# Performance work log

Measured on AMD Instinct MI355X. Metric: run time of the kernel, lower is better.

The kernel has to match this reference:

```python
import jax, jax.numpy as jnp
import numpy as np

N_NODES = 50000


def _build_graph(edge_index):
    # Add self-loops (PyG GCNConv default) and compute symmetric normalization.
    n = N_NODES
    loops = jnp.arange(n, dtype=edge_index.dtype)
    src = jnp.concatenate([edge_index[0], loops])
    dst = jnp.concatenate([edge_index[1], loops])
    deg = jax.ops.segment_sum(jnp.ones_like(dst, dtype=jnp.float32), dst, num_segments=n)
    dinv = jax.lax.rsqrt(jnp.maximum(deg, 1e-12))
    norm = dinv[src] * dinv[dst]  # [E+N]
    return src, dst, norm


def _gcn_layer(h, src, dst, norm, W, b):
    # transform-then-propagate: out[dst] += norm * (h @ W)[src]
    h = h @ W  # [N, D_out]
    msg = h[src] * norm[:, None]  # [E+N, D_out]
    agg = jax.ops.segment_sum(msg, dst, num_segments=N_NODES)
    return agg + b


def setup_inputs() -> dict:
    key = jax.random.key(0)
    ks = jax.random.split(key, 8)
    in_dim, hid, out = 128, 64, 32
    n_edges = 800000
    x = jax.random.normal(ks[0], (N_NODES, in_dim), dtype=jnp.float32)
    edge_index = jax.random.randint(ks[1], (2, n_edges), 0, N_NODES, dtype=jnp.int32)
    W1 = jax.random.normal(ks[2], (in_dim, hid), dtype=jnp.float32) / np.sqrt(in_dim)
    b1 = jnp.zeros((hid,), jnp.float32)
    W2 = jax.random.normal(ks[3], (hid, out), dtype=jnp.float32) / np.sqrt(hid)
    b2 = jnp.zeros((out,), jnp.float32)
    attn_w = jax.random.normal(ks[4], (out, 1), dtype=jnp.float32) / np.sqrt(out)
    attn_b = jnp.zeros((1,), jnp.float32)
    return {"x": x, "edge_index": edge_index, "W1": W1, "b1": b1,
            "W2": W2, "b2": b2, "attn_w": attn_w, "attn_b": attn_b}


def reference(x, edge_index, W1, b1, W2, b2, attn_w, attn_b):
    src, dst, norm = _build_graph(edge_index)
    h = jax.nn.relu(_gcn_layer(x, src, dst, norm, W1, b1))
    h = jax.nn.relu(_gcn_layer(h, src, dst, norm, W2, b2))
    attn = jax.nn.sigmoid(h @ attn_w + attn_b)  # [N, 1]
    return h * attn
```

## Files before the change

kernel.cpp:

```cpp
#include <hip/hip_runtime.h>
#include <hip/hip_fp16.h>
#include <math.h>

#define N_NODES 50000
#define SLICE_SZ 6250

__device__ __forceinline__ void fma4(float4& a, float w, const float4& v) {
    a.x += w * v.x; a.y += w * v.y; a.z += w * v.z; a.w += w * v.w;
}

struct h2x2 { __half2 a, b; };

__global__ void count_kernel(const int* __restrict__ dst, int E,
                             int* __restrict__ counts, int* __restrict__ rank) {
    int i = blockIdx.x * blockDim.x + threadIdx.x;
    if (i < E) rank[i] = atomicAdd(&counts[dst[i]], 1);
}

__global__ void scan_block_kernel(const int* __restrict__ in, int n,
                                  int* __restrict__ outEx, int* __restrict__ blocksum) {
    __shared__ int s[256];
    int t = threadIdx.x, i = blockIdx.x * 256 + t;
    int v = (i < n) ? in[i] : 0;
    s[t] = v;
    __syncthreads();
    for (int off = 1; off < 256; off <<= 1) {
        int x = (t >= off) ? s[t - off] : 0;
        __syncthreads();
        s[t] += x;
        __syncthreads();
    }
    if (i < n) outEx[i] = s[t] - v;
    if (t == 255 && blocksum) blocksum[blockIdx.x] = s[255];
}

__global__ void finalize_kernel(const int* __restrict__ counts, const int* __restrict__ blocksum,
                                int n, int E, int* __restrict__ row_ptr,
                                float* __restrict__ dinv) {
    int i = blockIdx.x * blockDim.x + threadIdx.x;
    if (i < n) {
        row_ptr[i] += blocksum[i >> 8];
        dinv[i] = rsqrtf((float)(counts[i] + 1));
        if (i == 0) row_ptr[n] = E;
    }
}

__global__ void fill2_kernel(const int* __restrict__ src, const int* __restrict__ dst,
                             const int* __restrict__ rank, int E,
                             const int* __restrict__ row_ptr, const float* __restrict__ dinv,
                             int2* __restrict__ edges) {
    const int slice = blockIdx.x & 7;
    const int chunk = blockIdx.x >> 3;
    const int CS = (((E + 255) >> 8) + 3) & ~3;
    const int lo = chunk * CS;
    const int hi = min(E, lo + CS);
    const int slo = slice * SLICE_SZ, shi = slo + SLICE_SZ;
    if (lo >= E) return;
    const int quad_end = lo + ((hi - lo) & ~3);
    for (int i = lo + threadIdx.x * 4; i + 3 < quad_end + 4 && i + 3 < hi + 4 && i < quad_end; i += 1024) {
        int4 d4 = *(const int4*)&dst[i];
        #pragma unroll
        for (int k = 0; k < 4; ++k) {
            int d = (&d4.x)[k];
            if (d >= slo && d < shi) {
                int s = src[i + k];
                int p = row_ptr[d] + rank[i + k];
                edges[p] = make_int2(s, __float_as_int(dinv[s] * dinv[d]));
            }
        }
    }
    for (int i = quad_end + threadIdx.x; i < hi; i += 256) {
        int d = dst[i];
        if (d >= slo && d < shi) {
            int s = src[i];
            int p = row_ptr[d] + rank[i];
            edges[p] = make_int2(s, __float_as_int(dinv[s] * dinv[d]));
        }
    }
}

template<int DIN, int DOUT, int BM, int KC, bool HOUT>
__global__ __launch_bounds__(256, 2) void gemm_kernel(const float* __restrict__ A,
                                                      const float* __restrict__ W,
                                                      void* __restrict__ Cv, int n) {
    constexpr int NCG = DOUT / 4;
    constexpr int NRG = BM / 4;
    static_assert(NCG * NRG == 256, "thread mapping");
    constexpr int KG = KC / 4;
    constexpr int RSTEP = 256 / KG;
    __shared__ __align__(16) float ws[DIN * DOUT];
    __shared__ __align__(16) float xs[KC][BM + 4];
    const int t = threadIdx.x;
    for (int i = 4 * t; i < DIN * DOUT; i += 1024)
        *(float4*)&ws[i] = *(const float4*)&W[i];
    const int rowbase = blockIdx.x * BM;
    const int r0 = (t / NCG) * 4;
    const int c0 = (t % NCG) * 4;
    const int lk = (t % KG) * 4;
    const int lr = t / KG;
    float acc[4][4] = {};
    for (int kc = 0; kc < DIN; kc += KC) {
        __syncthreads();
        #pragma unroll
        for (int r = lr; r < BM; r += RSTEP) {
            int row = rowbase + r;
            if (row >= n) row = n - 1;
            float4 v = *(const float4*)&A[(size_t)row * DIN + kc + lk];
            xs[lk + 0][r] = v.x; xs[lk + 1][r] = v.y;
            xs[lk + 2][r] = v.z; xs[lk + 3][r] = v.w;
        }
        __syncthreads();
        #pragma unroll 8
        for (int k = 0; k < KC; ++k) {
            float ar[4], wr[4];
            *(float4*)ar = *(const float4*)&xs[k][r0];
            *(float4*)wr = *(const float4*)&ws[(kc + k) * DOUT + c0];
            #pragma unroll
            for (int i = 0; i < 4; ++i)
                #pragma unroll
                for (int j = 0; j < 4; ++j)
                    acc[i][j] += ar[i] * wr[j];
        }
    }
    #pragma unroll
    for (int i = 0; i < 4; ++i) {
        int row = rowbase + r0 + i;
        if (row < n) {
            if constexpr (HOUT) {
                union { uint2 u; __half2 h[2]; } pk;
                pk.h[0] = __floats2half2_rn(acc[i][0], acc[i][1]);
                pk.h[1] = __floats2half2_rn(acc[i][2], acc[i][3]);
                *(uint2*)((__half*)Cv + (size_t)row * DOUT + c0) = pk.u;
            } else {
                float4 v = make_float4(acc[i][0], acc[i][1], acc[i][2], acc[i][3]);
                *(float4*)&((float*)Cv)[(size_t)row * DOUT + c0] = v;
            }
        }
    }
}

__global__ __launch_bounds__(256) void gather64_fuse_kernel(
        const __half* __restrict__ XWh, const int* __restrict__ row_ptr,
        const int2* __restrict__ edges, const float* __restrict__ dinv,
        const float* __restrict__ b1, const float* __restrict__ W2,
        float* __restrict__ out, int n) {
    __shared__ float ws2R[64 * 33];
    const int t = threadIdx.x;
    for (int i = t; i < 64 * 32; i += 256) {
        int f = i >> 5, j = i & 31;
        ws2R[f * 33 + (((j & 7) << 2) | (j >> 3))] = W2[i];
    }
    __syncthreads();
    const int node = blockIdx.x * 4 + (t >> 6);
    if (node >= n) return;
    const int lane = t & 63;
    const int fg = lane & 15, way = lane >> 4;
    const h2x2* __restrict__ XW4 = (const h2x2*)XWh;
    float4 acc = make_float4(0.f, 0.f, 0.f, 0.f);
    if (way == 0) {
        float dv = dinv[node];
        h2x2 r = XW4[(size_t)node * 16 + fg];
        float2 f0 = __half22float2(r.a), f1 = __half22float2(r.b);
        float s2 = dv * dv;
        acc.x = s2 * f0.x; acc.y = s2 * f0.y; acc.z = s2 * f1.x; acc.w = s2 * f1.y;
    }
    int e = row_ptr[node] + way;
    const int end = row_ptr[node + 1];
    for (; e + 4 < end; e += 8) {
        int2 p0 = edges[e], p1 = edges[e + 4];
        h2x2 r0 = XW4[(size_t)p0.x * 16 + fg];
        h2x2 r1 = XW4[(size_t)p1.x * 16 + fg];
        float w0 = __int_as_float(p0.y), w1 = __int_as_float(p1.y);
        float2 a0 = __half22float2(r0.a), b0 = __half22float2(r0.b);
        float2 a1 = __half22float2(r1.a), b1v = __half22float2(r1.b);
        acc.x += w0 * a0.x; acc.y += w0 * a0.y; acc.z += w0 * b0.x; acc.w += w0 * b0.y;
        acc.x += w1 * a1.x; acc.y += w1 * a1.y; acc.z += w1 * b1v.x; acc.w += w1 * b1v.y;
    }
    for (; e < end; e += 4) {
        int2 p = edges[e];
        h2x2 r = XW4[(size_t)p.x * 16 + fg];
        float w0 = __int_as_float(p.y);
        float2 a0 = __half22float2(r.a), b0 = __half22float2(r.b);
        acc.x += w0 * a0.x; acc.y += w0 * a0.y; acc.z += w0 * b0.x; acc.w += w0 * b0.y;
    }
    #pragma unroll
    for (int m = 16; m <= 32; m <<= 1) {
        acc.x += __shfl_xor(acc.x, m, 64);
        acc.y += __shfl_xor(acc.y, m, 64);
        acc.z += __shfl_xor(acc.z, m, 64);
        acc.w += __shfl_xor(acc.w, m, 64);
    }
    float4 b = ((const float4*)b1)[fg];
    float4 h;
    h.x = fmaxf(acc.x + b.x, 0.f);
    h.y = fmaxf(acc.y + b.y, 0.f);
    h.z = fmaxf(acc.z + b.z, 0.f);
    h.w = fmaxf(acc.w + b.w, 0.f);
    const int rbase = fg * 132;
    float py[8];
    #pragma unroll
    for (int s = 0; s < 8; ++s) {
        int idx = rbase + 4 * s + way;
        py[s] = h.x * ws2R[idx]
              + h.y * ws2R[idx + 33]
              + h.z * ws2R[idx + 66]
              + h.w * ws2R[idx + 99];
    }
    #pragma unroll
    for (int m = 1; m <= 8; m <<= 1) {
        #pragma unroll
        for (int s = 0; s < 8; ++s) py[s] += __shfl_xor(py[s], m, 64);
    }
    if (fg == 0) {
        float4* o = (float4*)&out[(size_t)node * 32 + way * 8];
        o[0] = make_float4(py[0], py[1], py[2], py[3]);
        o[1] = make_float4(py[4], py[5], py[6], py[7]);
    }
}

__global__ __launch_bounds__(256) void gather32_final_kernel(
        const float* __restrict__ XW, const int* __restrict__ row_ptr,
        const int2* __restrict__ edges, const float* __restrict__ dinv,
        const float* __restrict__ b2, const float* __restrict__ aw,
        const float* __restrict__ ab, float* __restrict__ out, int n) {
    const int t = threadIdx.x;
    const int node = blockIdx.x * 4 + (t >> 6);
    if (node >= n) return;
    const int lane = t & 63;
    const int fg = lane & 7, way = lane >> 3;
    const float4* __restrict__ XW4 = (const float4*)XW;
    float4 acc = make_float4(0.f, 0.f, 0.f, 0.f);
    if (way == 0) {
        float dv = dinv[node];
        float4 v = XW4[(size_t)node * 8 + fg];
        float s2 = dv * dv;
        acc.x = s2 * v.x; acc.y = s2 * v.y; acc.z = s2 * v.z; acc.w = s2 * v.w;
    }
    int e = row_ptr[node] + way;
    const int end = row_ptr[node + 1];
    for (; e + 8 < end; e += 16) {
        int2 p0 = edges[e], p1 = edges[e + 8];
        float4 v0 = XW4[(size_t)p0.x * 8 + fg];
        float4 v1 = XW4[(size_t)p1.x * 8 + fg];
        fma4(acc, __int_as_float(p0.y), v0);
        fma4(acc, __int_as_float(p1.y), v1);
    }
    for (; e < end; e += 8) {
        int2 p = edges[e];
        fma4(acc, __int_as_float(p.y), XW4[(size_t)p.x * 8 + fg]);
    }
    #pragma unroll
    for (int m = 8; m <= 32; m <<= 1) {
        acc.x += __shfl_xor(acc.x, m, 64);
        acc.y += __shfl_xor(acc.y, m, 64);
        acc.z += __shfl_xor(acc.z, m, 64);
        acc.w += __shfl_xor(acc.w, m, 64);
    }
    float4 b = ((const float4*)b2)[fg];
    float4 h;
    h.x = fmaxf(acc.x + b.x, 0.f);
    h.y = fmaxf(acc.y + b.y, 0.f);
    h.z = fmaxf(acc.z + b.z, 0.f);
    h.w = fmaxf(acc.w + b.w, 0.f);
    float4 a4 = ((const float4*)aw)[fg];
    float sca = h.x * a4.x + h.y * a4.y + h.z * a4.z + h.w * a4.w;
    sca += __shfl_xor(sca, 1, 64);
    sca += __shfl_xor(sca, 2, 64);
    sca += __shfl_xor(sca, 4, 64);
    float attn = 1.f / (1.f + __expf(-(sca + ab[0])));
    if (way == 0) {
        float4 r = make_float4(h.x * attn, h.y * attn, h.z * attn, h.w * attn);
        ((float4*)&out[(size_t)node * 32])[fg] = r;
    }
}

extern "C" void kernel_launch(void* const* d_in, const int* in_sizes, int n_in,
                              void* d_out, int out_size, void* d_ws, size_t ws_size,
                              hipStream_t stream) {
    const float* x  = (const float*)d_in[0];
    const int*   ei = (const int*)d_in[1];
    const float* W1 = (const float*)d_in[2];
    const float* b1 = (const float*)d_in[3];
    const float* W2 = (const float*)d_in[4];
    const float* b2 = (const float*)d_in[5];
    const float* aw = (const float*)d_in[6];
    const float* ab = (const float*)d_in[7];
    float* out = (float*)d_out;

    const int n = N_NODES;
    const int E = in_sizes[1] / 2;
    const int* src = ei;
    const int* dst = ei + E;

    char* w = (char*)d_ws;
    auto alloc = [&](size_t bytes) { char* p = w; w += (bytes + 255) & ~(size_t)255; return p; };
    int*    counts   = (int*)   alloc((size_t)n * 4);
    int*    row_ptr  = (int*)   alloc((size_t)(n + 1) * 4);
    int*    rank     = (int*)   alloc((size_t)E * 4);
    int*    blocksum = (int*)   alloc(1024);
    float*  dinv     = (float*) alloc((size_t)n * 4);
    int2*   edges    = (int2*)  alloc((size_t)E * 8);
    __half* bufAh    = (__half*)alloc((size_t)n * 64 * 2);
    float*  bufB     = (float*) alloc((size_t)n * 32 * 4);

    const int nb = (n + 255) / 256;

    hipMemsetAsync(counts, 0, (size_t)n * 4, stream);
    count_kernel<<<(E + 255) / 256, 256, 0, stream>>>(dst, E, counts, rank);
    scan_block_kernel<<<nb, 256, 0, stream>>>(counts, n, row_ptr, blocksum);
    scan_block_kernel<<<1, 256, 0, stream>>>(blocksum, nb, blocksum, nullptr);
    finalize_kernel<<<nb, 256, 0, stream>>>(counts, blocksum, n, E, row_ptr, dinv);
    fill2_kernel<<<256 * 8, 256, 0, stream>>>(src, dst, rank, E, row_ptr, dinv, edges);

    gemm_kernel<128, 64, 64, 32, true><<<(n + 63) / 64, 256, 0, stream>>>(x, W1, bufAh, n);
    gather64_fuse_kernel<<<(n + 3) / 4, 256, 0, stream>>>(
        bufAh, row_ptr, edges, dinv, b1, W2, bufB, n);
    gather32_final_kernel<<<(n + 3) / 4, 256, 0, stream>>>(
        bufB, row_ptr, edges, dinv, b2, aw, ab, out, n);
}
```

Measured before the change: 247.8 us.

## Stage edge records via wavefront shuffle and process four nodes per wave

Each wavefront now loads up to 64 edge records (plus a self-loop record) for a node in one coalesced load. It then broadcasts source index and weight with shuffles instead of having each lane group load edges separately. Each wave loops over four nodes, so a block covers 16 nodes, which amortises the W2 shared-memory staging in the first gather kernel. Padding lanes use zero weights with the node's own row, which adds some wasted gathers for low-degree nodes. The grid is correspondingly reduced fourfold.

```diff
diff --git a/kernel.cpp b/kernel.cpp
--- a/kernel.cpp
+++ b/kernel.cpp
@@ -151,70 +151,81 @@
         ws2R[f * 33 + (((j & 7) << 2) | (j >> 3))] = W2[i];
     }
     __syncthreads();
-    const int node = blockIdx.x * 4 + (t >> 6);
-    if (node >= n) return;
     const int lane = t & 63;
+    const int wid = t >> 6;
     const int fg = lane & 15, way = lane >> 4;
     const h2x2* __restrict__ XW4 = (const h2x2*)XWh;
-    float4 acc = make_float4(0.f, 0.f, 0.f, 0.f);
-    if (way == 0) {
-        float dv = dinv[node];
-        h2x2 r = XW4[(size_t)node * 16 + fg];
-        float2 f0 = __half22float2(r.a), f1 = __half22float2(r.b);
-        float s2 = dv * dv;
-        acc.x = s2 * f0.x; acc.y = s2 * f0.y; acc.z = s2 * f1.x; acc.w = s2 * f1.y;
-    }
-    int e = row_ptr[node] + way;
-    const int end = row_ptr[node + 1];
-    for (; e + 4 < end; e += 8) {
-        int2 p0 = edges[e], p1 = edges[e + 4];
-        h2x2 r0 = XW4[(size_t)p0.x * 16 + fg];
-        h2x2 r1 = XW4[(size_t)p1.x * 16 + fg];
-        float w0 = __int_as_float(p0.y), w1 = __int_as_float(p1.y);
-        float2 a0 = __half22float2(r0.a), b0 = __half22float2(r0.b);
-        float2 a1 = __half22float2(r1.a), b1v = __half22float2(r1.b);
-        acc.x += w0 * a0.x; acc.y += w0 * a0.y; acc.z += w0 * b0.x; acc.w += w0 * b0.y;
-        acc.x += w1 * a1.x; acc.y += w1 * a1.y; acc.z += w1 * b1v.x; acc.w += w1 * b1v.y;
-    }
-    for (; e < end; e += 4) {
-        int2 p = edges[e];
-        h2x2 r = XW4[(size_t)p.x * 16 + fg];
-        float w0 = __int_as_float(p.y);
-        float2 a0 = __half22float2(r.a), b0 = __half22float2(r.b);
-        acc.x += w0 * a0.x; acc.y += w0 * a0.y; acc.z += w0 * b0.x; acc.w += w0 * b0.y;
-    }
-    #pragma unroll
-    for (int m = 16; m <= 32; m <<= 1) {
-        acc.x += __shfl_xor(acc.x, m, 64);
-        acc.y += __shfl_xor(acc.y, m, 64);
-        acc.z += __shfl_xor(acc.z, m, 64);
-        acc.w += __shfl_xor(acc.w, m, 64);
-    }
-    float4 b = ((const float4*)b1)[fg];
-    float4 h;
-    h.x = fmaxf(acc.x + b.x, 0.f);
-    h.y = fmaxf(acc.y + b.y, 0.f);
-    h.z = fmaxf(acc.z + b.z, 0.f);
-    h.w = fmaxf(acc.w + b.w, 0.f);
-    const int rbase = fg * 132;
-    float py[8];
-    #pragma unroll
-    for (int s = 0; s < 8; ++s) {
-        int idx = rbase + 4 * s + way;
-        py[s] = h.x * ws2R[idx]
-              + h.y * ws2R[idx + 33]
-              + h.z * ws2R[idx + 66]
-              + h.w * ws2R[idx + 99];
-    }
-    #pragma unroll
-    for (int m = 1; m <= 8; m <<= 1) {
-        #pragma unroll
-        for (int s = 0; s < 8; ++s) py[s] += __shfl_xor(py[s], m, 64);
-    }
-    if (fg == 0) {
-        float4* o = (float4*)&out[(size_t)node * 32 + way * 8];
-        o[0] = make_float4(py[0], py[1], py[2], py[3]);
-        o[1] = make_float4(py[4], py[5], py[6], py[7]);
+    for (int it = 0; it < 4; ++it) {
+        const int node = blockIdx.x * 16 + wid * 4 + it;
+        if (node >= n) break;
+        const int start = row_ptr[node];
+        const int deg = row_ptr[node + 1] - start;
+        const int K = deg + 1;
+        int2 rec;
+        if (lane == 0) {
+            float dv = dinv[node];
+            rec = make_int2(node, __float_as_int(dv * dv));
+        } else if (lane <= deg) {
+            rec = edges[start + lane - 1];
+        } else {
+            rec = make_int2(node, 0);
+        }
+        float4 acc = make_float4(0.f, 0.f, 0.f, 0.f);
+        const int KP = (min(K, 64) + 3) & ~3;
+        int k = way;
+        #define G64_STEP(kk)                                                   \
+            { int sv = __shfl(rec.x, (kk), 64);                                \
+              float wgt = __int_as_float(__shfl(rec.y, (kk), 64));             \
+              h2x2 rr = XW4[(size_t)sv * 16 + fg];                             \
+              float2 a0 = __half22float2(rr.a), b0 = __half22float2(rr.b);     \
+              acc.x += wgt * a0.x; acc.y += wgt * a0.y;                        \
+              acc.z += wgt * b0.x; acc.w += wgt * b0.y; }
+        for (; k + 12 < KP; k += 16) {
+            G64_STEP(k) G64_STEP(k + 4) G64_STEP(k + 8) G64_STEP(k + 12)
+        }
+        for (; k < KP; k += 4) G64_STEP(k)
+        #undef G64_STEP
+        for (int kk = 64 + way; kk < K; kk += 4) {
+            int2 p = edges[start + kk - 1];
+            float wgt = __int_as_float(p.y);
+            h2x2 rr = XW4[(size_t)p.x * 16 + fg];
+            float2 a0 = __half22float2(rr.a), b0 = __half22float2(rr.b);
+            acc.x += wgt * a0.x; acc.y += wgt * a0.y;
+            acc.z += wgt * b0.x; acc.w += wgt * b0.y;
+        }
+        #pragma unroll
+        for (int m = 16; m <= 32; m <<= 1) {
+            acc.x += __shfl_xor(acc.x, m, 64);
+            acc.y += __shfl_xor(acc.y, m, 64);
+            acc.z += __shfl_xor(acc.z, m, 64);
+            acc.w += __shfl_xor(acc.w, m, 64);
+        }
+        float4 b = ((const float4*)b1)[fg];
+        float4 h;
+        h.x = fmaxf(acc.x + b.x, 0.f);
+        h.y = fmaxf(acc.y + b.y, 0.f);
+        h.z = fmaxf(acc.z + b.z, 0.f);
+        h.w = fmaxf(acc.w + b.w, 0.f);
+        const int rbase = fg * 132;
+        float py[8];
+        #pragma unroll
+        for (int s = 0; s < 8; ++s) {
+            int idx = rbase + 4 * s + way;
+            py[s] = h.x * ws2R[idx]
+                  + h.y * ws2R[idx + 33]
+                  + h.z * ws2R[idx + 66]
+                  + h.w * ws2R[idx + 99];
+        }
+        #pragma unroll
+        for (int m = 1; m <= 8; m <<= 1) {
+            #pragma unroll
+            for (int s = 0; s < 8; ++s) py[s] += __shfl_xor(py[s], m, 64);
+        }
+        if (fg == 0) {
+            float4* o = (float4*)&out[(size_t)node * 32 + way * 8];
+            o[0] = make_float4(py[0], py[1], py[2], py[3]);
+            o[1] = make_float4(py[4], py[5], py[6], py[7]);
+        }
     }
 }
 
@@ -224,53 +235,65 @@
         const float* __restrict__ b2, const float* __restrict__ aw,
         const float* __restrict__ ab, float* __restrict__ out, int n) {
     const int t = threadIdx.x;
-    const int node = blockIdx.x * 4 + (t >> 6);
-    if (node >= n) return;
     const int lane = t & 63;
+    const int wid = t >> 6;
     const int fg = lane & 7, way = lane >> 3;
     const float4* __restrict__ XW4 = (const float4*)XW;
-    float4 acc = make_float4(0.f, 0.f, 0.f, 0.f);
-    if (way == 0) {
-        float dv = dinv[node];
-        float4 v = XW4[(size_t)node * 8 + fg];
-        float s2 = dv * dv;
-        acc.x = s2 * v.x; acc.y = s2 * v.y; acc.z = s2 * v.z; acc.w = s2 * v.w;
-    }
-    int e = row_ptr[node] + way;
-    const int end = row_ptr[node + 1];
-    for (; e + 8 < end; e += 16) {
-        int2 p0 = edges[e], p1 = edges[e + 8];
-        float4 v0 = XW4[(size_t)p0.x * 8 + fg];
-        float4 v1 = XW4[(size_t)p1.x * 8 + fg];
-        fma4(acc, __int_as_float(p0.y), v0);
-        fma4(acc, __int_as_float(p1.y), v1);
-    }
-    for (; e < end; e += 8) {
-        int2 p = edges[e];
-        fma4(acc, __int_as_float(p.y), XW4[(size_t)p.x * 8 + fg]);
-    }
-    #pragma unroll
-    for (int m = 8; m <= 32; m <<= 1) {
-        acc.x += __shfl_xor(acc.x, m, 64);
-        acc.y += __shfl_xor(acc.y, m, 64);
-        acc.z += __shfl_xor(acc.z, m, 64);
-        acc.w += __shfl_xor(acc.w, m, 64);
-    }
-    float4 b = ((const float4*)b2)[fg];
-    float4 h;
-    h.x = fmaxf(acc.x + b.x, 0.f);
-    h.y = fmaxf(acc.y + b.y, 0.f);
-    h.z = fmaxf(acc.z + b.z, 0.f);
-    h.w = fmaxf(acc.w + b.w, 0.f);
-    float4 a4 = ((const float4*)aw)[fg];
-    float sca = h.x * a4.x + h.y * a4.y + h.z * a4.z + h.w * a4.w;
-    sca += __shfl_xor(sca, 1, 64);
-    sca += __shfl_xor(sca, 2, 64);
-    sca += __shfl_xor(sca, 4, 64);
-    float attn = 1.f / (1.f + __expf(-(sca + ab[0])));
-    if (way == 0) {
-        float4 r = make_float4(h.x * attn, h.y * attn, h.z * attn, h.w * attn);
-        ((float4*)&out[(size_t)node * 32])[fg] = r;
+    for (int it = 0; it < 4; ++it) {
+        const int node = blockIdx.x * 16 + wid * 4 + it;
+        if (node >= n) break;
+        const int start = row_ptr[node];
+        const int deg = row_ptr[node + 1] - start;
+        const int K = deg + 1;
+        int2 rec;
+        if (lane == 0) {
+            float dv = dinv[node];
+            rec = make_int2(node, __float_as_int(dv * dv));
+        } else if (lane <= deg) {
+            rec = edges[start + lane - 1];
+        } else {
+            rec = make_int2(node, 0);
+        }
+        float4 acc = make_float4(0.f, 0.f, 0.f, 0.f);
+        const int KP = (min(K, 64) + 7) & ~7;
+        int k = way;
+        #define G32_STEP(kk)                                                   \
+            { int sv = __shfl(rec.x, (kk), 64);                                \
+              float wgt = __int_as_float(__shfl(rec.y, (kk), 64));             \
+              float4 v = XW4[(size_t)sv * 8 + fg];                             \
+              fma4(acc, wgt, v); }
+        for (; k + 24 < KP; k += 32) {
+            G32_STEP(k) G32_STEP(k + 8) G32_STEP(k + 16) G32_STEP(k + 24)
+        }
+        for (; k < KP; k += 8) G32_STEP(k)
+        #undef G32_STEP
+        for (int kk = 64 + way; kk < K; kk += 8) {
+            int2 p = edges[start + kk - 1];
+            fma4(acc, __int_as_float(p.y), XW4[(size_t)p.x * 8 + fg]);
+        }
+        #pragma unroll
+        for (int m = 8; m <= 32; m <<= 1) {
+            acc.x += __shfl_xor(acc.x, m, 64);
+            acc.y += __shfl_xor(acc.y, m, 64);
+            acc.z += __shfl_xor(acc.z, m, 64);
+            acc.w += __shfl_xor(acc.w, m, 64);
+        }
+        float4 b = ((const float4*)b2)[fg];
+        float4 h;
+        h.x = fmaxf(acc.x + b.x, 0.f);
+        h.y = fmaxf(acc.y + b.y, 0.f);
+        h.z = fmaxf(acc.z + b.z, 0.f);
+        h.w = fmaxf(acc.w + b.w, 0.f);
+        float4 a4 = ((const float4*)aw)[fg];
+        float sca = h.x * a4.x + h.y * a4.y + h.z * a4.z + h.w * a4.w;
+        sca += __shfl_xor(sca, 1, 64);
+        sca += __shfl_xor(sca, 2, 64);
+        sca += __shfl_xor(sca, 4, 64);
+        float attn = 1.f / (1.f + __expf(-(sca + ab[0])));
+        if (way == 0) {
+            float4 r = make_float4(h.x * attn, h.y * attn, h.z * attn, h.w * attn);
+            ((float4*)&out[(size_t)node * 32])[fg] = r;
+        }
     }
 }
 
@@ -313,8 +336,8 @@
     fill2_kernel<<<256 * 8, 256, 0, stream>>>(src, dst, rank, E, row_ptr, dinv, edges);
 
     gemm_kernel<128, 64, 64, 32, true><<<(n + 63) / 64, 256, 0, stream>>>(x, W1, bufAh, n);
-    gather64_fuse_kernel<<<(n + 3) / 4, 256, 0, stream>>>(
+    gather64_fuse_kernel<<<(n + 15) / 16, 256, 0, stream>>>(
         bufAh, row_ptr, edges, dinv, b1, W2, bufB, n);
-    gather32_final_kernel<<<(n + 3) / 4, 256, 0, stream>>>(
+    gather32_final_kernel<<<(n + 15) / 16, 256, 0, stream>>>(
         bufB, row_ptr, edges, dinv, b2, aw, ab, out, n);
 }
```

Result: faster. 237.4 us (-4.2%).
